# Kernel tuning notes

Measured on AMD Instinct MI355X. Metric: run time of the kernel, lower is better.

## Reference

```python
import jax, jax.numpy as jnp
import numpy as np

OUT_F, IN_F = 4096, 11008
NUMEL = OUT_F * IN_F            # divisible by 256
NUM_SUPER = NUMEL // 256        # super-blocks of 8 sub-blocks x 32 values


def setup_inputs() -> dict:
    key = jax.random.key(0)
    k = jax.random.split(key, 7)
    x = jax.random.normal(k[0], (64, IN_F), dtype=jnp.float32)
    packed = jax.random.randint(k[1], (NUMEL // 2,), 0, 256, dtype=jnp.int32)
    d = jax.random.uniform(k[2], (NUM_SUPER,), dtype=jnp.float32) * 0.02
    dmin = jax.random.uniform(k[3], (NUM_SUPER,), dtype=jnp.float32) * 0.02
    scales = jax.random.randint(k[4], (NUM_SUPER * 8,), 0, 64, dtype=jnp.int32)
    mins = jax.random.randint(k[5], (NUM_SUPER * 8,), 0, 64, dtype=jnp.int32)
    bias = jax.random.normal(k[6], (OUT_F,), dtype=jnp.float32) * 0.02
    return {"x": x, "packed": packed, "d": d, "dmin": dmin,
            "scales": scales, "mins": mins, "bias": bias}


def _dequant_q4k(packed, d, dmin, scales, mins):
    # unpack two 4-bit quants per byte, interleaved low/high (stack dim=1 + flatten)
    low = packed & 15
    high = (packed >> 4) & 15
    q = jnp.stack([low, high], axis=1).reshape(NUM_SUPER, 8, 32).astype(jnp.float32)
    sc = (scales.astype(jnp.float32) / 63.0).reshape(NUM_SUPER, 8, 1)
    mn = (mins.astype(jnp.float32) / 63.0).reshape(NUM_SUPER, 8, 1)
    normalized = q / 15.0 * sc + mn
    w = normalized * d.reshape(NUM_SUPER, 1, 1) + dmin.reshape(NUM_SUPER, 1, 1)
    return w.reshape(OUT_F, IN_F)


def reference(x, packed, d, dmin, scales, mins, bias):
    w = _dequant_q4k(packed, d, dmin, scales, mins)   # [OUT_F, IN_F] fp32
    return x @ w.T + bias                              # F.linear
```

## Files before the change

### kernel.cpp

```cpp
#include <hip/hip_runtime.h>
#include <stdint.h>

#define OUT_F   4096
#define IN_F    11008
#define BATCH   64
#define NSUP    43
#define SB_ROW  344
#define IPR     5504
#define NKS     8
#define NCB     64
#define XP_BYTES   (344 * 256 * 16)
#define SCMN_BYTES (NSUP * 4096 * 16)
#define DDM_BYTES  (NSUP * 4096 * 8)
#define PART_OFF   (XP_BYTES + SCMN_BYTES + DDM_BYTES)
#define PART_BYTES ((size_t)NKS * BATCH * OUT_F * 4)
#define WS_FULL    (PART_OFF + PART_BYTES)

typedef __attribute__((ext_vector_type(8))) short  short8;
typedef __attribute__((ext_vector_type(4))) float  floatx4;
typedef __attribute__((ext_vector_type(4))) int    intx4;

__device__ __forceinline__ unsigned pack_bf16(float f0, float f1) {
    return __builtin_amdgcn_perm(__float_as_uint(f1), __float_as_uint(f0), 0x07060302u);
}

__global__ __launch_bounds__(256) void prep_kernel(const float* __restrict__ x,
                                                   const int* __restrict__ scales,
                                                   const int* __restrict__ mins,
                                                   const float* __restrict__ dd,
                                                   const float* __restrict__ dmn,
                                                   intx4* __restrict__ xp,
                                                   intx4* __restrict__ scmn_p,
                                                   float2* __restrict__ ddm_p) {
    if (blockIdx.x < 344) {
        const int ksb = blockIdx.x;
        const int mt  = threadIdx.x >> 6;
        const int l   = threadIdx.x & 63;
        const int lo  = l & 15, hi = l >> 4;
        const float* src = x + (mt * 16 + lo) * IN_F + ksb * 32 + hi * 8;
        floatx4 a0 = *(const floatx4*)src;
        floatx4 a1 = *(const floatx4*)(src + 4);
        intx4 r;
        r.x = pack_bf16(a0.x, a0.y);
        r.y = pack_bf16(a0.z, a0.w);
        r.z = pack_bf16(a1.x, a1.y);
        r.w = pack_bf16(a1.z, a1.w);
        xp[(mt * 344 + ksb) * 64 + l] = r;
    } else {
        const int tg  = (blockIdx.x - 344) * 256 + threadIdx.x;
        const int row = tg / 43;
        const int sup = tg - row * 43;
        const intx4 s0 = *(const intx4*)(scales + row * SB_ROW + sup * 8);
        const intx4 s1 = *(const intx4*)(scales + row * SB_ROW + sup * 8 + 4);
        const intx4 m0 = *(const intx4*)(mins   + row * SB_ROW + sup * 8);
        const intx4 m1 = *(const intx4*)(mins   + row * SB_ROW + sup * 8 + 4);
        intx4 o;
        o.x = s0.x | (s0.y << 8) | (s0.z << 16) | (s0.w << 24);
        o.y = s1.x | (s1.y << 8) | (s1.z << 16) | (s1.w << 24);
        o.z = m0.x | (m0.y << 8) | (m0.z << 16) | (m0.w << 24);
        o.w = m1.x | (m1.y << 8) | (m1.z << 16) | (m1.w << 24);
        scmn_p[sup * 4096 + row] = o;
        float2 dp;
        dp.x = dd[row * NSUP + sup];
        dp.y = dmn[row * NSUP + sup];
        ddm_p[sup * 4096 + row] = dp;
    }
}

__global__ __launch_bounds__(256) void init_out_kernel(const float* __restrict__ bias,
                                                       float* __restrict__ out) {
    int i = blockIdx.x * 256 + threadIdx.x;
    out[i] = bias[i & (OUT_F - 1)];
}

__global__ __launch_bounds__(256) void reduce_kernel(const float* __restrict__ part,
                                                     const float* __restrict__ bias,
                                                     float* __restrict__ out) {
    const int i = blockIdx.x * 256 + threadIdx.x;
    float s = bias[i & (OUT_F - 1)];
    #pragma unroll
    for (int k = 0; k < NKS; ++k) s += part[(size_t)k * (BATCH * OUT_F) + i];
    out[i] = s;
}

template<bool USE_PART>
__global__ __launch_bounds__(256, 2) void qlin_main(
    const intx4*  __restrict__ xp,
    const int*    __restrict__ packed,
    const intx4*  __restrict__ scmn_p,
    const float2* __restrict__ ddm_p,
    float*        __restrict__ part,
    float*        __restrict__ out)
{
    __shared__ int    wds[64 * 132];
    __shared__ intx4  xfs[2048];
    __shared__ intx4  scs[64];
    __shared__ float2 dds[64];

    const int ks  = blockIdx.x & 7;
    const int nb  = blockIdx.x >> 3;
    const int tid = threadIdx.x;
    const int w   = tid >> 6;
    const int l   = tid & 63;
    const int lo  = l & 15, hi = l >> 4;

    const int sup0 = ks < 3 ? 6 * ks : 18 + 5 * (ks - 3);
    const int nsup = ks < 3 ? 6 : 5;

    const int srow = w * 16 + (l >> 5);
    const int schk = l & 31;
    const int* gb0 = packed + (nb * 64 + srow) * IPR + schk * 4;

    floatx4 acc[4];
    #pragma unroll
    for (int mt = 0; mt < 4; ++mt) acc[mt] = (floatx4)0.0f;

    const int myrow = w * 16 + lo;

    #pragma unroll 1
    for (int s = 0; s < nsup; ++s) {
        const int sup = sup0 + s;
        __syncthreads();

        intx4 wtmp[8];
        const int* gb = gb0 + sup * 128;
        #pragma unroll
        for (int i = 0; i < 8; ++i)
            wtmp[i] = *(const intx4*)(gb + 2 * i * IPR);

        intx4 xtmp[8];
        const intx4* xsrc = xp + sup * 512;
        #pragma unroll
        for (int i = 0; i < 8; ++i) {
            const int idx = i * 256 + tid;
            xtmp[i] = xsrc[(idx >> 9) * 22016 + (idx & 511)];
        }
        intx4 sctv; float2 ddv;
        if (tid < 64)       sctv = scmn_p[sup * 4096 + nb * 64 + tid];
        else if (tid < 128) ddv  = ddm_p[sup * 4096 + nb * 64 + (tid - 64)];

        #pragma unroll
        for (int i = 0; i < 8; ++i)
            *(intx4*)&wds[(srow + 2 * i) * 132 + schk * 4] = wtmp[i];
        #pragma unroll
        for (int i = 0; i < 8; ++i)
            xfs[i * 256 + tid] = xtmp[i];
        if (tid < 64)       scs[tid] = sctv;
        else if (tid < 128) dds[tid - 64] = ddv;
        __syncthreads();

        const intx4  sv = scs[myrow];
        const float2 dp = dds[myrow];
        const float a945 = dp.x * (1.0f / 945.0f);
        const float a63  = dp.x * (1.0f / 63.0f);

        #pragma unroll
        for (int st = 0; st < 8; ++st) {
            const intx4 bv = *(const intx4*)&wds[myrow * 132 + st * 16 + hi * 4];
            const int scw = (st < 4) ? sv.x : sv.y;
            const int mnw = (st < 4) ? sv.z : sv.w;
            const float A = a945 * (float)((scw >> ((st & 3) * 8)) & 255);
            const float B = fmaf(a63, (float)((mnw >> ((st & 3) * 8)) & 255), dp.y);

            union { intx4 i; short8 s8; } uw;
            uw.i.x = pack_bf16(fmaf((float)(bv.x & 15), A, B),
                               fmaf((float)(bv.x >> 4), A, B));
            uw.i.y = pack_bf16(fmaf((float)(bv.y & 15), A, B),
                               fmaf((float)(bv.y >> 4), A, B));
            uw.i.z = pack_bf16(fmaf((float)(bv.z & 15), A, B),
                               fmaf((float)(bv.z >> 4), A, B));
            uw.i.w = pack_bf16(fmaf((float)(bv.w & 15), A, B),
                               fmaf((float)(bv.w >> 4), A, B));

            union { intx4 i; short8 s8; } u0, u1, u2, u3;
            u0.i = xfs[0 * 512 + st * 64 + l];
            u1.i = xfs[1 * 512 + st * 64 + l];
            u2.i = xfs[2 * 512 + st * 64 + l];
            u3.i = xfs[3 * 512 + st * 64 + l];
            acc[0] = __builtin_amdgcn_mfma_f32_16x16x32_bf16(u0.s8, uw.s8, acc[0], 0, 0, 0);
            acc[1] = __builtin_amdgcn_mfma_f32_16x16x32_bf16(u1.s8, uw.s8, acc[1], 0, 0, 0);
            acc[2] = __builtin_amdgcn_mfma_f32_16x16x32_bf16(u2.s8, uw.s8, acc[2], 0, 0, 0);
            acc[3] = __builtin_amdgcn_mfma_f32_16x16x32_bf16(u3.s8, uw.s8, acc[3], 0, 0, 0);
        }
    }

    const int o = nb * 64 + myrow;
    if (USE_PART) {
        float* p0 = part + (size_t)ks * (BATCH * OUT_F) + o;
        #pragma unroll
        for (int mt = 0; mt < 4; ++mt) {
            #pragma unroll
            for (int r = 0; r < 4; ++r)
                p0[(mt * 16 + hi * 4 + r) * OUT_F] = acc[mt][r];
        }
    } else {
        #pragma unroll
        for (int mt = 0; mt < 4; ++mt) {
            #pragma unroll
            for (int r = 0; r < 4; ++r)
                atomicAdd(out + (mt * 16 + hi * 4 + r) * OUT_F + o, acc[mt][r]);
        }
    }
}

extern "C" void kernel_launch(void* const* d_in, const int* in_sizes, int n_in,
                              void* d_out, int out_size, void* d_ws, size_t ws_size,
                              hipStream_t stream) {
    (void)in_sizes; (void)n_in; (void)out_size;
    const float* x      = (const float*)d_in[0];
    const int*   packed = (const int*)d_in[1];
    const float* d      = (const float*)d_in[2];
    const float* dmin   = (const float*)d_in[3];
    const int*   scales = (const int*)d_in[4];
    const int*   mins   = (const int*)d_in[5];
    const float* bias   = (const float*)d_in[6];
    float* out = (float*)d_out;

    intx4*  xp     = (intx4*)d_ws;
    intx4*  scmn_p = (intx4*)((char*)d_ws + XP_BYTES);
    float2* ddm_p  = (float2*)((char*)d_ws + XP_BYTES + SCMN_BYTES);
    float*  part   = (float*)((char*)d_ws + PART_OFF);
    const bool has_part = ws_size >= (size_t)WS_FULL;

    prep_kernel<<<344 + 688, 256, 0, stream>>>(x, scales, mins, d, dmin, xp, scmn_p, ddm_p);

    if (has_part) {
        qlin_main<true><<<NCB * NKS, 256, 0, stream>>>(
            xp, packed, scmn_p, ddm_p, part, out);
        reduce_kernel<<<(BATCH * OUT_F) / 256, 256, 0, stream>>>(part, bias, out);
    } else {
        init_out_kernel<<<(BATCH * OUT_F) / 256, 256, 0, stream>>>(bias, out);
        qlin_main<false><<<NCB * NKS, 256, 0, stream>>>(
            xp, packed, scmn_p, ddm_p, part, out);
    }
}
```

Baseline: 169.8 us.

## Repack int32 nibbles into compact MFMA-ordered weight buffer in prep kernel

Adds a repack stage to the prep kernel that compresses the int32-per-byte packed weights into 4-bit nibbles, laid out in the exact per-lane MFMA fragment order. The main kernel then loads two 16-byte vectors per lane per super-block straight into registers, dropping the LDS weight staging and the bank-padded shared buffer. The cost is an extra full read of the packed input plus a write and re-read of the compact buffer on every call, plus a larger workspace requirement.

Measured after the change: 175.2 us. +3.1%, slower.

```diff
diff --git a/kernel.cpp b/kernel.cpp
--- a/kernel.cpp
+++ b/kernel.cpp
@@ -12,9 +12,12 @@
 #define XP_BYTES   (344 * 256 * 16)
 #define SCMN_BYTES (NSUP * 4096 * 16)
 #define DDM_BYTES  (NSUP * 4096 * 8)
-#define PART_OFF   (XP_BYTES + SCMN_BYTES + DDM_BYTES)
+#define PW_OFF     (XP_BYTES + SCMN_BYTES + DDM_BYTES)
+#define PW_REAL    ((size_t)OUT_F * IN_F / 2)
+#define PART_OFF   (PW_OFF + PW_REAL)
 #define PART_BYTES ((size_t)NKS * BATCH * OUT_F * 4)
 #define WS_FULL    (PART_OFF + PART_BYTES)
+#define REPACK_BLKS 11008
 
 typedef __attribute__((ext_vector_type(8))) short  short8;
 typedef __attribute__((ext_vector_type(4))) float  floatx4;
@@ -24,16 +27,39 @@
     return __builtin_amdgcn_perm(__float_as_uint(f1), __float_as_uint(f0), 0x07060302u);
 }
 
+__device__ __forceinline__ unsigned low_bytes4(intx4 d) {
+    unsigned p01 = __builtin_amdgcn_perm((unsigned)d.y, (unsigned)d.x, 0x00000400u);
+    unsigned p23 = __builtin_amdgcn_perm((unsigned)d.w, (unsigned)d.z, 0x00000400u);
+    return __builtin_amdgcn_perm(p23, p01, 0x05040100u);
+}
+
 __global__ __launch_bounds__(256) void prep_kernel(const float* __restrict__ x,
+                                                   const int* __restrict__ packed,
                                                    const int* __restrict__ scales,
                                                    const int* __restrict__ mins,
                                                    const float* __restrict__ dd,
                                                    const float* __restrict__ dmn,
                                                    intx4* __restrict__ xp,
+                                                   int2* __restrict__ pw,
                                                    intx4* __restrict__ scmn_p,
                                                    float2* __restrict__ ddm_p) {
-    if (blockIdx.x < 344) {
-        const int ksb = blockIdx.x;
+    if (blockIdx.x < REPACK_BLKS) {
+        const int gid  = blockIdx.x * 256 + threadIdx.x;
+        const int st2  = gid & 3;
+        const int lane = (gid >> 2) & 63;
+        const int gs   = gid >> 8;
+        const int lo   = lane & 15, hi = lane >> 4;
+        const int row  = (gs / 43) * 16 + lo;
+        const int sup  = gs % 43;
+        const int base = row * IPR + sup * 128 + st2 * 32 + hi * 4;
+        intx4 d0 = *(const intx4*)(packed + base);
+        intx4 d1 = *(const intx4*)(packed + base + 16);
+        int2 o;
+        o.x = (int)low_bytes4(d0);
+        o.y = (int)low_bytes4(d1);
+        pw[gid] = o;
+    } else if (blockIdx.x < REPACK_BLKS + 344) {
+        const int ksb = blockIdx.x - REPACK_BLKS;
         const int mt  = threadIdx.x >> 6;
         const int l   = threadIdx.x & 63;
         const int lo  = l & 15, hi = l >> 4;
@@ -47,7 +73,7 @@
         r.w = pack_bf16(a1.z, a1.w);
         xp[(mt * 344 + ksb) * 64 + l] = r;
     } else {
-        const int tg  = (blockIdx.x - 344) * 256 + threadIdx.x;
+        const int tg  = (blockIdx.x - REPACK_BLKS - 344) * 256 + threadIdx.x;
         const int row = tg / 43;
         const int sup = tg - row * 43;
         const intx4 s0 = *(const intx4*)(scales + row * SB_ROW + sup * 8);
@@ -86,13 +112,12 @@
 template<bool USE_PART>
 __global__ __launch_bounds__(256, 2) void qlin_main(
     const intx4*  __restrict__ xp,
-    const int*    __restrict__ packed,
+    const intx4*  __restrict__ pw4,
     const intx4*  __restrict__ scmn_p,
     const float2* __restrict__ ddm_p,
     float*        __restrict__ part,
     float*        __restrict__ out)
 {
-    __shared__ int    wds[64 * 132];
     __shared__ intx4  xfs[2048];
     __shared__ intx4  scs[64];
     __shared__ float2 dds[64];
@@ -106,10 +131,7 @@
 
     const int sup0 = ks < 3 ? 6 * ks : 18 + 5 * (ks - 3);
     const int nsup = ks < 3 ? 6 : 5;
-
-    const int srow = w * 16 + (l >> 5);
-    const int schk = l & 31;
-    const int* gb0 = packed + (nb * 64 + srow) * IPR + schk * 4;
+    const int g    = nb * 4 + w;
 
     floatx4 acc[4];
     #pragma unroll
@@ -122,11 +144,9 @@
         const int sup = sup0 + s;
         __syncthreads();
 
-        intx4 wtmp[8];
-        const int* gb = gb0 + sup * 128;
-        #pragma unroll
-        for (int i = 0; i < 8; ++i)
-            wtmp[i] = *(const intx4*)(gb + 2 * i * IPR);
+        const intx4* wp = pw4 + ((size_t)(g * 43 + sup) * 64 + l) * 2;
+        intx4 w8a = wp[0];
+        intx4 w8b = wp[1];
 
         intx4 xtmp[8];
         const intx4* xsrc = xp + sup * 512;
@@ -139,9 +159,6 @@
         if (tid < 64)       sctv = scmn_p[sup * 4096 + nb * 64 + tid];
         else if (tid < 128) ddv  = ddm_p[sup * 4096 + nb * 64 + (tid - 64)];
 
-        #pragma unroll
-        for (int i = 0; i < 8; ++i)
-            *(intx4*)&wds[(srow + 2 * i) * 132 + schk * 4] = wtmp[i];
         #pragma unroll
         for (int i = 0; i < 8; ++i)
             xfs[i * 256 + tid] = xtmp[i];
@@ -156,21 +173,21 @@
 
         #pragma unroll
         for (int st = 0; st < 8; ++st) {
-            const intx4 bv = *(const intx4*)&wds[myrow * 132 + st * 16 + hi * 4];
+            const unsigned u = (unsigned)((st < 4) ? w8a[st] : w8b[st - 4]);
             const int scw = (st < 4) ? sv.x : sv.y;
             const int mnw = (st < 4) ? sv.z : sv.w;
             const float A = a945 * (float)((scw >> ((st & 3) * 8)) & 255);
             const float B = fmaf(a63, (float)((mnw >> ((st & 3) * 8)) & 255), dp.y);
 
             union { intx4 i; short8 s8; } uw;
-            uw.i.x = pack_bf16(fmaf((float)(bv.x & 15), A, B),
-                               fmaf((float)(bv.x >> 4), A, B));
-            uw.i.y = pack_bf16(fmaf((float)(bv.y & 15), A, B),
-                               fmaf((float)(bv.y >> 4), A, B));
-            uw.i.z = pack_bf16(fmaf((float)(bv.z & 15), A, B),
-                               fmaf((float)(bv.z >> 4), A, B));
-            uw.i.w = pack_bf16(fmaf((float)(bv.w & 15), A, B),
-                               fmaf((float)(bv.w >> 4), A, B));
+            uw.i.x = pack_bf16(fmaf((float)(u & 15u), A, B),
+                               fmaf((float)((u >> 4) & 15u), A, B));
+            uw.i.y = pack_bf16(fmaf((float)((u >> 8) & 15u), A, B),
+                               fmaf((float)((u >> 12) & 15u), A, B));
+            uw.i.z = pack_bf16(fmaf((float)((u >> 16) & 15u), A, B),
+                               fmaf((float)((u >> 20) & 15u), A, B));
+            uw.i.w = pack_bf16(fmaf((float)((u >> 24) & 15u), A, B),
+                               fmaf((float)(u >> 28), A, B));
 
             union { intx4 i; short8 s8; } u0, u1, u2, u3;
             u0.i = xfs[0 * 512 + st * 64 + l];
@@ -219,18 +236,20 @@
     intx4*  xp     = (intx4*)d_ws;
     intx4*  scmn_p = (intx4*)((char*)d_ws + XP_BYTES);
     float2* ddm_p  = (float2*)((char*)d_ws + XP_BYTES + SCMN_BYTES);
+    int2*   pw     = (int2*)((char*)d_ws + PW_OFF);
     float*  part   = (float*)((char*)d_ws + PART_OFF);
     const bool has_part = ws_size >= (size_t)WS_FULL;
 
-    prep_kernel<<<344 + 688, 256, 0, stream>>>(x, scales, mins, d, dmin, xp, scmn_p, ddm_p);
+    prep_kernel<<<REPACK_BLKS + 344 + 688, 256, 0, stream>>>(
+        x, packed, scales, mins, d, dmin, xp, pw, scmn_p, ddm_p);
 
     if (has_part) {
         qlin_main<true><<<NCB * NKS, 256, 0, stream>>>(
-            xp, packed, scmn_p, ddm_p, part, out);
+            xp, (const intx4*)pw, scmn_p, ddm_p, part, out);
         reduce_kernel<<<(BATCH * OUT_F) / 256, 256, 0, stream>>>(part, bias, out);
     } else {
         init_out_kernel<<<(BATCH * OUT_F) / 256, 256, 0, stream>>>(bias, out);
         qlin_main<false><<<NCB * NKS, 256, 0, stream>>>(
-            xp, packed, scmn_p, ddm_p, part, out);
-    }
-}
+            xp, (const intx4*)pw, scmn_p, ddm_p, part, out);
+    }
+}
```
